# Optimization experiments

Measured on AMD Instinct MI355X. Metric: run time of the kernel, lower is better.

The kernel has to match this reference:

```python
import jax, jax.numpy as jnp
import numpy as np

jax.config.update("jax_enable_x64", True)

EPS = 1e-5
ENERGY_THRESH = 0.95
N_, C_, H_, W_ = 64, 64, 64, 64


def setup_inputs() -> dict:
    key = jax.random.key(0)
    k1, k2 = jax.random.split(key)
    x = jax.random.normal(k1, (N_, C_, H_, W_), dtype=jnp.float32)
    weight = jax.random.uniform(k2, (C_, 1), dtype=jnp.float32)
    bias = jnp.zeros((C_, 1), dtype=jnp.float32)
    return {"x": x, "weight": weight, "bias": bias}


def reference(x, weight, bias):
    # Training path of myZCANorm (the expensive, kernel-relevant branch).
    N, C, H, W = x.shape
    n_eigens = C // 2
    f64 = jnp.float64
    xd = x.astype(f64).transpose(1, 0, 2, 3).reshape(C, -1)  # [C, NHW]
    mu = xd.mean(1, keepdims=True)
    var = jnp.var(xd, axis=1, ddof=1, keepdims=True)  # torch.var is unbiased
    xh = (xd - mu) / jnp.sqrt(var + EPS)
    M0 = xh @ xh.T / (N * H * W) + EPS * jnp.eye(C, dtype=f64)  # [C, C] covariance

    # torch.svd under no_grad: eigen-init + ground-truth energies (no gradient)
    e, V = jnp.linalg.eigh(jax.lax.stop_gradient(M0))
    e = e[::-1]            # descending eigenvalues
    V = V[:, ::-1]
    cum_energy = jnp.cumsum(e) / jnp.sum(e)
    stop_after = cum_energy >= ENERGY_THRESH  # loop breaks AFTER using index i

    def step(carry, i):
        M, done, Wxr = carry
        active = ~done
        v0 = V[:, i]
        Mv = M @ v0                      # one power-iteration step (power_iteration_once)
        v = Mv / jnp.linalg.norm(Mv)
        lam = v @ (M @ v)                # Rayleigh quotient eigenvalue
        a = active.astype(f64)
        vvT = jnp.outer(v, v)
        Wxr = Wxr + a * vvT / jnp.sqrt(lam)
        done_new = done | stop_after[i]
        deflate = (active & ~stop_after[i]).astype(f64)
        M = M - deflate * jnp.outer(M @ v, v)  # deflation: M -= (M v) v^T
        return (M, done_new, Wxr), None

    init = (M0, jnp.array(False), jnp.zeros((C, C), dtype=f64))
    (_, _, Wxr), _ = jax.lax.scan(step, init, jnp.arange(n_eigens))

    # xr.T = sum_i (x^T v_i / sqrt(lam_i)) v_i^T  ->  xr = Wxr @ xh  (Wxr symmetric)
    out = Wxr @ xh                                   # [C, NHW]
    out = out * weight.astype(f64) + bias.astype(f64)
    out = out.reshape(C, N, H, W).transpose(1, 0, 2, 3)
    return out.astype(jnp.float32)
```

## Files before the change

kernel.cpp:

```cpp
#include <hip/hip_runtime.h>


__global__ __launch_bounds__(256) void zca_zero_k(double* __restrict__ p) {
  for (int i = threadIdx.x; i < 4160; i += 256) p[i] = 0.0;
}

__global__ __launch_bounds__(256) void zca_gram_k(const float* __restrict__ x,
                                                  double* __restrict__ S,
                                                  double* __restrict__ rowsum) {
  __shared__ float XT[128 * 72];
  const int t = threadIdx.x;
  const int n = blockIdx.x >> 3;
  const int k0base = (blockIdx.x & 7) << 9;
  const float* xb = x + ((size_t)n << 18);
  const int cg = t >> 4, dg = t & 15;
  const int sc = t & 63, kq = t >> 6;

  double acc[4][4];
#pragma unroll
  for (int i = 0; i < 4; ++i)
#pragma unroll
    for (int j = 0; j < 4; ++j) acc[i][j] = 0.0;
  double rs[4] = {0.0, 0.0, 0.0, 0.0};

  for (int tile = 0; tile < 4; ++tile) {
    const int k0 = k0base + (tile << 7);
#pragma unroll
    for (int r = 0; r < 8; ++r) {
      const int kk = ((kq << 3) + r) << 2;
      const float4 v = *reinterpret_cast<const float4*>(xb + ((size_t)sc << 12) + k0 + kk);
      XT[(kk + 0) * 72 + sc] = v.x;
      XT[(kk + 1) * 72 + sc] = v.y;
      XT[(kk + 2) * 72 + sc] = v.z;
      XT[(kk + 3) * 72 + sc] = v.w;
    }
    __syncthreads();
    float accf[4][4];
#pragma unroll
    for (int i = 0; i < 4; ++i)
#pragma unroll
      for (int j = 0; j < 4; ++j) accf[i][j] = 0.0f;
    float rsf[4] = {0.f, 0.f, 0.f, 0.f};
#pragma unroll 2
    for (int kk = 0; kk < 128; ++kk) {
      const float4 a4 = *reinterpret_cast<const float4*>(XT + kk * 72 + (cg << 2));
      const float4 b4 = *reinterpret_cast<const float4*>(XT + kk * 72 + (dg << 2));
      const float a[4] = {a4.x, a4.y, a4.z, a4.w};
      const float b[4] = {b4.x, b4.y, b4.z, b4.w};
#pragma unroll
      for (int i = 0; i < 4; ++i) {
#pragma unroll
        for (int j = 0; j < 4; ++j) accf[i][j] = fmaf(a[i], b[j], accf[i][j]);
        rsf[i] += a[i];
      }
    }
#pragma unroll
    for (int i = 0; i < 4; ++i) {
#pragma unroll
      for (int j = 0; j < 4; ++j) acc[i][j] += (double)accf[i][j];
      rs[i] += (double)rsf[i];
    }
    __syncthreads();
  }
  const int c0 = cg << 2, d0 = dg << 2;
#pragma unroll
  for (int i = 0; i < 4; ++i)
#pragma unroll
    for (int j = 0; j < 4; ++j)
      atomicAdd(&S[(c0 + i) * 64 + d0 + j], acc[i][j]);
  if (dg == 0) {
#pragma unroll
    for (int i = 0; i < 4; ++i) atomicAdd(&rowsum[c0 + i], rs[i]);
  }
}

__device__ __forceinline__ void zca_sched(int j, int r, int& p, int& q) {
  if (j == 0) {
    p = 0;
    int a = 62 + r; if (a >= 63) a -= 63;
    q = 1 + a;
  } else {
    int a = j - 1 + r;  if (a >= 63) a -= 63;
    int b = 62 - j + r; if (b >= 63) b -= 63;
    p = 1 + a;
    q = 1 + b;
  }
}

__global__ __launch_bounds__(256) void zca_solve_k(const double* __restrict__ S,
                                                   const double* __restrict__ rowsum,
                                                   const float* __restrict__ weight,
                                                   const float* __restrict__ bias,
                                                   float* __restrict__ T,
                                                   float* __restrict__ offv) {
  __shared__ __align__(16) float G[64 * 68];
  __shared__ float norms[64];
  __shared__ float lam[64];
  __shared__ float msd[64];
  __shared__ float isg[64];
  __shared__ double mu[64], sig[64];
  __shared__ float wk2[64];
  __shared__ int idxs[64];
  const int t = threadIdx.x;
  const double n = 262144.0;

  if (t < 64) {
    const double m = rowsum[t] / n;
    const double var = (S[t * 64 + t] - n * m * m) / (n - 1.0);
    mu[t] = m;
    sig[t] = sqrt(var + 1e-5);
    msd[t] = (float)(m / sig[t]);
    isg[t] = (float)(1.0 / sig[t]);
  }
  __syncthreads();
  for (int e = t; e < 4096; e += 256) {
    const int col = e >> 6, row = e & 63;
    double v = (S[row * 64 + col] - n * mu[row] * mu[col]) / (n * sig[row] * sig[col]);
    if (row == col) v += 1e-5;
    G[col * 68 + row] = (float)v;
  }
  __syncthreads();
  if (t < 64) {
    float s = 0.0f;
#pragma unroll
    for (int j4 = 0; j4 < 16; ++j4) {
      const float4 v = *reinterpret_cast<const float4*>(G + t * 68 + (j4 << 2));
      s = fmaf(v.x, v.x, s); s = fmaf(v.y, v.y, s);
      s = fmaf(v.z, v.z, s); s = fmaf(v.w, v.w, s);
    }
    norms[t] = s;
  }
  __syncthreads();

  if (t < 64) {
    const int g = t >> 1;
    const int o = (t & 1) << 5;
    for (int sweep = 0; sweep < 8; ++sweep) {
      int anyflag = 0;
      for (int round = 0; round < 63; ++round) {
        int p, q;
        zca_sched(g, round, p, q);
        float* Gp = G + p * 68 + o;
        float* Gq = G + q * 68 + o;
        float4 P[8], Q[8];
#pragma unroll
        for (int i = 0; i < 8; ++i) P[i] = *reinterpret_cast<float4*>(Gp + (i << 2));
#pragma unroll
        for (int i = 0; i < 8; ++i) Q[i] = *reinterpret_cast<float4*>(Gq + (i << 2));
        float apq = 0.0f;
#pragma unroll
        for (int i = 0; i < 8; ++i) {
          apq = fmaf(P[i].x, Q[i].x, apq);
          apq = fmaf(P[i].y, Q[i].y, apq);
          apq = fmaf(P[i].z, Q[i].z, apq);
          apq = fmaf(P[i].w, Q[i].w, apq);
        }
        apq += __shfl_xor(apq, 1);
        const float app = norms[p], aqq = norms[q];
        if (apq * apq > 1e-11f * app * aqq) {
          anyflag = 1;
          const float tau = (aqq - app) / (2.0f * apq);
          const float tt = (tau >= 0.0f ? 1.0f : -1.0f) / (fabsf(tau) + sqrtf(1.0f + tau * tau));
          const float c = 1.0f / sqrtf(1.0f + tt * tt);
          const float s = tt * c;
#pragma unroll
          for (int i = 0; i < 8; ++i) {
            float4 np, nq;
            np.x = c * P[i].x - s * Q[i].x; np.y = c * P[i].y - s * Q[i].y;
            np.z = c * P[i].z - s * Q[i].z; np.w = c * P[i].w - s * Q[i].w;
            nq.x = s * P[i].x + c * Q[i].x; nq.y = s * P[i].y + c * Q[i].y;
            nq.z = s * P[i].z + c * Q[i].z; nq.w = s * P[i].w + c * Q[i].w;
            *reinterpret_cast<float4*>(Gp + (i << 2)) = np;
            *reinterpret_cast<float4*>(Gq + (i << 2)) = nq;
          }
          if ((t & 1) == 0) norms[p] = app - tt * apq;
          else              norms[q] = aqq + tt * apq;
        }
        __builtin_amdgcn_wave_barrier();
      }
      if (!__any(anyflag)) break;
    }
  }
  __syncthreads();

  if (t < 64) {
    float s = 0.0f;
#pragma unroll
    for (int j4 = 0; j4 < 16; ++j4) {
      const float4 v = *reinterpret_cast<const float4*>(G + t * 68 + (j4 << 2));
      s = fmaf(v.x, v.x, s); s = fmaf(v.y, v.y, s);
      s = fmaf(v.z, v.z, s); s = fmaf(v.w, v.w, s);
    }
    lam[t] = sqrtf(s);
  }
  __syncthreads();
  if (t < 64) {
    const float e = lam[t];
    int rank = 0;
    for (int j = 0; j < 64; ++j) {
      const float ej = lam[j];
      if (ej > e || (ej == e && j < t)) ++rank;
    }
    idxs[rank] = t;
  }
  __syncthreads();
  if (t == 0) {
    double total = 0.0;
    for (int j = 0; j < 64; ++j) total += (double)lam[j];
    double cum = 0.0;
    bool done = false;
    for (int k = 0; k < 64; ++k) {
      const double l = (double)lam[idxs[k]];
      cum += l;
      double w = 0.0;
      if (k < 32 && !done) w = 1.0 / (sqrt(l) * l * l);
      if (cum / total >= 0.95) done = true;
      wk2[k] = (float)w;
    }
  }
  __syncthreads();
  {
    const int c = t >> 2, db = (t & 3) << 4;
    float accf[16];
#pragma unroll
    for (int d = 0; d < 16; ++d) accf[d] = 0.0f;
    for (int k = 0; k < 32; ++k) {
      const int sk = idxs[k];
      const float vc = wk2[k] * G[sk * 68 + c];
      const float* gcol = G + sk * 68 + db;
#pragma unroll
      for (int d4 = 0; d4 < 4; ++d4) {
        const float4 v = *reinterpret_cast<const float4*>(gcol + (d4 << 2));
        accf[d4 * 4 + 0] = fmaf(vc, v.x, accf[d4 * 4 + 0]);
        accf[d4 * 4 + 1] = fmaf(vc, v.y, accf[d4 * 4 + 1]);
        accf[d4 * 4 + 2] = fmaf(vc, v.z, accf[d4 * 4 + 2]);
        accf[d4 * 4 + 3] = fmaf(vc, v.w, accf[d4 * 4 + 3]);
      }
    }
    const float wc = weight[c];
    float po = 0.0f;
#pragma unroll
    for (int d = 0; d < 16; ++d) {
      T[c * 64 + db + d] = wc * accf[d] * isg[db + d];
      po = fmaf(accf[d], msd[db + d], po);
    }
    po += __shfl_xor(po, 1);
    po += __shfl_xor(po, 2);
    if ((t & 3) == 0) offv[c] = bias[c] - wc * po;
  }
}

__global__ __launch_bounds__(256) void zca_apply_k(const float* __restrict__ x,
                                                   const float* __restrict__ T,
                                                   const float* __restrict__ offv,
                                                   float* __restrict__ out) {
  __shared__ __align__(16) float4 Tl4[64 * 16];
  __shared__ float offl[64];
  const int t = threadIdx.x;
  for (int e = t; e < 1024; e += 256) Tl4[e] = reinterpret_cast<const float4*>(T)[e];
  if (t < 64) offl[t] = offv[t];
  __syncthreads();
  const int n = blockIdx.x >> 3;
  const int k0 = ((blockIdx.x & 7) << 9) + (t << 1);
  const float* xb = x + ((size_t)n << 18) + k0;
  float2 acc[64];
#pragma unroll
  for (int c = 0; c < 64; ++c) { acc[c].x = offl[c]; acc[c].y = offl[c]; }
  float2 xv[4];
#pragma unroll
  for (int dd = 0; dd < 4; ++dd)
    xv[dd] = *reinterpret_cast<const float2*>(xb + ((size_t)dd << 12));
  for (int d4 = 0; d4 < 16; ++d4) {
    float2 xn[4];
    if (d4 < 15) {
#pragma unroll
      for (int dd = 0; dd < 4; ++dd)
        xn[dd] = *reinterpret_cast<const float2*>(xb + ((size_t)((d4 + 1) * 4 + dd) << 12));
    }
#pragma unroll
    for (int c = 0; c < 64; ++c) {
      const float4 tv = Tl4[(c << 4) + d4];
      acc[c].x = fmaf(tv.x, xv[0].x, acc[c].x); acc[c].y = fmaf(tv.x, xv[0].y, acc[c].y);
      acc[c].x = fmaf(tv.y, xv[1].x, acc[c].x); acc[c].y = fmaf(tv.y, xv[1].y, acc[c].y);
      acc[c].x = fmaf(tv.z, xv[2].x, acc[c].x); acc[c].y = fmaf(tv.z, xv[2].y, acc[c].y);
      acc[c].x = fmaf(tv.w, xv[3].x, acc[c].x); acc[c].y = fmaf(tv.w, xv[3].y, acc[c].y);
    }
#pragma unroll
    for (int dd = 0; dd < 4; ++dd) xv[dd] = xn[dd];
  }
  float* ob = out + ((size_t)n << 18) + k0;
#pragma unroll
  for (int c = 0; c < 64; ++c)
    *reinterpret_cast<float2*>(ob + ((size_t)c << 12)) = acc[c];
}

extern "C" void kernel_launch(void* const* d_in, const int* in_sizes, int n_in,
                              void* d_out, int out_size, void* d_ws, size_t ws_size,
                              hipStream_t stream) {
  const float* x = (const float*)d_in[0];
  const float* weight = (const float*)d_in[1];
  const float* bias = (const float*)d_in[2];
  float* out = (float*)d_out;
  char* ws = (char*)d_ws;
  double* S = (double*)ws;
  double* rowsum = (double*)(ws + 32768);
  float* T = (float*)(ws + 33280);
  float* offv = (float*)(ws + 49664);

  hipLaunchKernelGGL(zca_zero_k, dim3(1), dim3(256), 0, stream, S);
  hipLaunchKernelGGL(zca_gram_k, dim3(512), dim3(256), 0, stream, x, S, rowsum);
  hipLaunchKernelGGL(zca_solve_k, dim3(1), dim3(256), 0, stream, S, rowsum, weight, bias, T, offv);
  hipLaunchKernelGGL(zca_apply_k, dim3(512), dim3(256), 0, stream, x, T, offv, out);
}
```

Baseline: 473.2 us.

## Keep one-sided Jacobi columns in registers and exchange partners via wave shuffles

The single-block Jacobi eigen-solver now has each of 64 lanes hold one full column of G in 64 registers. Partner columns are fetched with __shfl, replacing the previous scheme of two lanes per pair reading and writing shared memory with wave barriers. Column norms are tracked per lane in a register instead of a shared array. The maximum sweep count drops from 8 to 7, and the zeroing kernel is replaced by hipMemsetAsync. This aims to cut LDS traffic and latency in the serial solve, at the cost of high register pressure (64 shuffles per round) and one fewer allowed sweep.

```diff
diff --git a/kernel.cpp b/kernel.cpp
--- a/kernel.cpp
+++ b/kernel.cpp
@@ -1,9 +1,5 @@
 #include <hip/hip_runtime.h>
 
-
-__global__ __launch_bounds__(256) void zca_zero_k(double* __restrict__ p) {
-  for (int i = threadIdx.x; i < 4160; i += 256) p[i] = 0.0;
-}
 
 __global__ __launch_bounds__(256) void zca_gram_k(const float* __restrict__ x,
                                                   double* __restrict__ S,
@@ -74,19 +70,6 @@
   }
 }
 
-__device__ __forceinline__ void zca_sched(int j, int r, int& p, int& q) {
-  if (j == 0) {
-    p = 0;
-    int a = 62 + r; if (a >= 63) a -= 63;
-    q = 1 + a;
-  } else {
-    int a = j - 1 + r;  if (a >= 63) a -= 63;
-    int b = 62 - j + r; if (b >= 63) b -= 63;
-    p = 1 + a;
-    q = 1 + b;
-  }
-}
-
 __global__ __launch_bounds__(256) void zca_solve_k(const double* __restrict__ S,
                                                    const double* __restrict__ rowsum,
                                                    const float* __restrict__ weight,
@@ -94,7 +77,6 @@
                                                    float* __restrict__ T,
                                                    float* __restrict__ offv) {
   __shared__ __align__(16) float G[64 * 68];
-  __shared__ float norms[64];
   __shared__ float lam[64];
   __shared__ float msd[64];
   __shared__ float isg[64];
@@ -120,80 +102,79 @@
     G[col * 68 + row] = (float)v;
   }
   __syncthreads();
+
   if (t < 64) {
-    float s = 0.0f;
-#pragma unroll
-    for (int j4 = 0; j4 < 16; ++j4) {
-      const float4 v = *reinterpret_cast<const float4*>(G + t * 68 + (j4 << 2));
-      s = fmaf(v.x, v.x, s); s = fmaf(v.y, v.y, s);
-      s = fmaf(v.z, v.z, s); s = fmaf(v.w, v.w, s);
-    }
-    norms[t] = s;
-  }
-  __syncthreads();
-
-  if (t < 64) {
-    const int g = t >> 1;
-    const int o = (t & 1) << 5;
-    for (int sweep = 0; sweep < 8; ++sweep) {
+    float C[64];
+#pragma unroll
+    for (int i4 = 0; i4 < 16; ++i4) {
+      const float4 v = *reinterpret_cast<const float4*>(G + t * 68 + (i4 << 2));
+      C[4 * i4 + 0] = v.x; C[4 * i4 + 1] = v.y;
+      C[4 * i4 + 2] = v.z; C[4 * i4 + 3] = v.w;
+    }
+    float nrm = 0.0f;
+#pragma unroll
+    for (int i = 0; i < 64; ++i) nrm = fmaf(C[i], C[i], nrm);
+
+    for (int sweep = 0; sweep < 7; ++sweep) {
       int anyflag = 0;
-      for (int round = 0; round < 63; ++round) {
-        int p, q;
-        zca_sched(g, round, p, q);
-        float* Gp = G + p * 68 + o;
-        float* Gq = G + q * 68 + o;
-        float4 P[8], Q[8];
-#pragma unroll
-        for (int i = 0; i < 8; ++i) P[i] = *reinterpret_cast<float4*>(Gp + (i << 2));
-#pragma unroll
-        for (int i = 0; i < 8; ++i) Q[i] = *reinterpret_cast<float4*>(Gq + (i << 2));
-        float apq = 0.0f;
-#pragma unroll
-        for (int i = 0; i < 8; ++i) {
-          apq = fmaf(P[i].x, Q[i].x, apq);
-          apq = fmaf(P[i].y, Q[i].y, apq);
-          apq = fmaf(P[i].z, Q[i].z, apq);
-          apq = fmaf(P[i].w, Q[i].w, apq);
+      for (int r = 0; r < 63; ++r) {
+        int partner, rolep;
+        if (t == 0) {
+          int pp = 62 + r; if (pp >= 63) pp -= 63;
+          partner = 1 + pp; rolep = 1;
+        } else {
+          int a = t - 1 - r; if (a < 0) a += 63;
+          if (a == 62) { partner = 0; rolep = 0; }
+          else {
+            int pp = 61 - a + r; if (pp >= 63) pp -= 63;
+            partner = 1 + pp;
+            rolep = (a <= 30) ? 1 : 0;
+          }
         }
-        apq += __shfl_xor(apq, 1);
-        const float app = norms[p], aqq = norms[q];
+        const float pn = __shfl(nrm, partner);
+        float Q[64];
+#pragma unroll
+        for (int i = 0; i < 64; ++i) Q[i] = __shfl(C[i], partner);
+        float s0 = 0.f, s1 = 0.f, s2 = 0.f, s3 = 0.f;
+#pragma unroll
+        for (int i = 0; i < 64; i += 4) {
+          s0 = fmaf(C[i + 0], Q[i + 0], s0);
+          s1 = fmaf(C[i + 1], Q[i + 1], s1);
+          s2 = fmaf(C[i + 2], Q[i + 2], s2);
+          s3 = fmaf(C[i + 3], Q[i + 3], s3);
+        }
+        const float apq = (s0 + s1) + (s2 + s3);
+        const float app = rolep ? nrm : pn;
+        const float aqq = rolep ? pn : nrm;
         if (apq * apq > 1e-11f * app * aqq) {
           anyflag = 1;
           const float tau = (aqq - app) / (2.0f * apq);
           const float tt = (tau >= 0.0f ? 1.0f : -1.0f) / (fabsf(tau) + sqrtf(1.0f + tau * tau));
           const float c = 1.0f / sqrtf(1.0f + tt * tt);
-          const float s = tt * c;
-#pragma unroll
-          for (int i = 0; i < 8; ++i) {
-            float4 np, nq;
-            np.x = c * P[i].x - s * Q[i].x; np.y = c * P[i].y - s * Q[i].y;
-            np.z = c * P[i].z - s * Q[i].z; np.w = c * P[i].w - s * Q[i].w;
-            nq.x = s * P[i].x + c * Q[i].x; nq.y = s * P[i].y + c * Q[i].y;
-            nq.z = s * P[i].z + c * Q[i].z; nq.w = s * P[i].w + c * Q[i].w;
-            *reinterpret_cast<float4*>(Gp + (i << 2)) = np;
-            *reinterpret_cast<float4*>(Gq + (i << 2)) = nq;
-          }
-          if ((t & 1) == 0) norms[p] = app - tt * apq;
-          else              norms[q] = aqq + tt * apq;
+          const float ts = rolep ? -tt : tt;
+          const float b = ts * c;
+          nrm = fmaf(ts, apq, nrm);
+#pragma unroll
+          for (int i = 0; i < 64; ++i) C[i] = fmaf(c, C[i], b * Q[i]);
         }
-        __builtin_amdgcn_wave_barrier();
       }
       if (!__any(anyflag)) break;
     }
-  }
-  __syncthreads();
-
-  if (t < 64) {
-    float s = 0.0f;
-#pragma unroll
-    for (int j4 = 0; j4 < 16; ++j4) {
-      const float4 v = *reinterpret_cast<const float4*>(G + t * 68 + (j4 << 2));
-      s = fmaf(v.x, v.x, s); s = fmaf(v.y, v.y, s);
-      s = fmaf(v.z, v.z, s); s = fmaf(v.w, v.w, s);
-    }
-    lam[t] = sqrtf(s);
-  }
-  __syncthreads();
+
+    float sn = 0.0f;
+#pragma unroll
+    for (int i = 0; i < 64; ++i) sn = fmaf(C[i], C[i], sn);
+    lam[t] = sqrtf(sn);
+#pragma unroll
+    for (int i4 = 0; i4 < 16; ++i4) {
+      float4 v;
+      v.x = C[4 * i4 + 0]; v.y = C[4 * i4 + 1];
+      v.z = C[4 * i4 + 2]; v.w = C[4 * i4 + 3];
+      *reinterpret_cast<float4*>(G + t * 68 + (i4 << 2)) = v;
+    }
+  }
+  __syncthreads();
+
   if (t < 64) {
     const float e = lam[t];
     int rank = 0;
@@ -307,7 +288,7 @@
   float* T = (float*)(ws + 33280);
   float* offv = (float*)(ws + 49664);
 
-  hipLaunchKernelGGL(zca_zero_k, dim3(1), dim3(256), 0, stream, S);
+  hipMemsetAsync(S, 0, 33280, stream);
   hipLaunchKernelGGL(zca_gram_k, dim3(512), dim3(256), 0, stream, x, S, rowsum);
   hipLaunchKernelGGL(zca_solve_k, dim3(1), dim3(256), 0, stream, S, rowsum, weight, bias, T, offv);
   hipLaunchKernelGGL(zca_apply_k, dim3(512), dim3(256), 0, stream, x, T, offv, out);
```

Measured after the change: 688.6 us. 45.5% more time.
